# Optimization experiments

Measured on AMD Instinct MI355X. Metric: run time of the kernel, lower is better.

Reference implementation:

```python
import jax, jax.numpy as jnp
import numpy as np

B, L, D, H = 2, 2048, 2048, 16
DH = D // H
SCALE = 1.0 / float(np.sqrt(DH))


def setup_inputs() -> dict:
    key = jax.random.key(0)
    ks = jax.random.split(key, 5)
    std = 1.0 / float(np.sqrt(D))
    return {
        "x": jax.random.normal(ks[0], (B, L, D), dtype=jnp.float32),
        "W_q": jax.random.normal(ks[1], (D, D), dtype=jnp.float32) * std,
        "W_k": jax.random.normal(ks[2], (D, D), dtype=jnp.float32) * std,
        "W_v": jax.random.normal(ks[3], (D, D), dtype=jnp.float32) * std,
        "W_o": jax.random.normal(ks[4], (D, D), dtype=jnp.float32) * std,
    }


def _split_heads(t):
    # (B, L, D) -> (B, H, L, DH)
    b, l, _ = t.shape
    return t.reshape(b, l, H, DH).transpose(0, 2, 1, 3)


def reference(x, W_q, W_k, W_v, W_o):
    # nn.Linear(bias=False): y = x @ W.T
    q = _split_heads(x @ W_q.T)  # (B,H,L,DH)
    k = _split_heads(x @ W_k.T)
    v = _split_heads(x @ W_v.T)
    scores = jnp.einsum("bhqd,bhkd->bhqk", q, k) * SCALE  # (B,H,L,L)
    causal = jnp.arange(L)[:, None] >= jnp.arange(L)[None, :]  # True = keep
    scores = jnp.where(causal[None, None], scores, -jnp.inf)
    attn = jax.nn.softmax(scores, axis=-1)
    y = jnp.einsum("bhqk,bhkd->bhqd", attn, v)  # (B,H,L,DH)
    y = y.transpose(0, 2, 1, 3).reshape(B, L, D)  # merge heads
    return y @ W_o.T
```

## Files before the change

kernel.cpp:

```cpp
#include <hip/hip_runtime.h>
#include <hip/hip_bf16.h>
#include <stdint.h>

typedef unsigned short u16;
typedef __bf16 bf16x8 __attribute__((ext_vector_type(8)));
typedef float f32x4 __attribute__((ext_vector_type(4)));

#define SEQ    2048
#define DMODEL 2048
#define NHEAD  16
#define DHEAD  128
#define QSCALE (0.088388347648318447f * 1.4426950408889634f)

__device__ __forceinline__ u16 f2bf(float f){
  uint32_t u = __float_as_uint(f);
  u += 0x7FFFu + ((u >> 16) & 1u);
  return (u16)(u >> 16);
}

__device__ __forceinline__ void gload_lds16(const u16* g, u16* l){
  __builtin_amdgcn_global_load_lds((const __attribute__((address_space(1))) void*)g,
                                   (__attribute__((address_space(3))) void*)l,
                                   16, 0, 0);
}

__global__ __launch_bounds__(256) void cvt_bf16(const float* __restrict__ src,
                                                u16* __restrict__ dst, int n4){
  int i = blockIdx.x * 256 + threadIdx.x;
  if (i < n4){
    float4 v = reinterpret_cast<const float4*>(src)[i];
    ushort4 o;
    o.x = f2bf(v.x); o.y = f2bf(v.y); o.z = f2bf(v.z); o.w = f2bf(v.w);
    reinterpret_cast<ushort4*>(dst)[i] = o;
  }
}

__global__ __launch_bounds__(256) void cvt_w4(const float* __restrict__ Wq,
    const float* __restrict__ Wk, const float* __restrict__ Wv,
    const float* __restrict__ Wo, u16* __restrict__ dst){
  const int z = blockIdx.y;
  const float* s = (z==0) ? Wq : (z==1) ? Wk : (z==2) ? Wv : Wo;
  int i = blockIdx.x * 256 + threadIdx.x;
  float4 v = reinterpret_cast<const float4*>(s)[i];
  ushort4 o;
  o.x = f2bf(v.x); o.y = f2bf(v.y); o.z = f2bf(v.z); o.w = f2bf(v.w);
  reinterpret_cast<ushort4*>(dst + (size_t)z*4194304)[i] = o;
}

__device__ __forceinline__ void stageA(const u16* __restrict__ G, int grow0, int kt,
                                       int half, u16* lds, int w, int lane){
  #pragma unroll
  for (int j = 0; j < 2; ++j){
    int q   = w*2 + j;
    int r0  = ((q & 8) << 4) + half*64 + (q & 7)*8;
    int row = r0 + (lane >> 3);
    int sc  = (lane & 7) ^ (row & 7);
    gload_lds16(G + (size_t)(grow0 + row)*DMODEL + kt*64 + sc*8, lds + r0*64);
  }
}
__device__ __forceinline__ void stageB(const u16* __restrict__ G, int grow0, int kt,
                                       int half, u16* lds, int w, int lane){
  #pragma unroll
  for (int j = 0; j < 2; ++j){
    int q   = w*2 + j;
    int r0  = ((q >> 2) << 6) + half*32 + (q & 3)*8;
    int row = r0 + (lane >> 3);
    int sc  = (lane & 7) ^ (row & 7);
    gload_lds16(G + (size_t)(grow0 + row)*DMODEL + kt*64 + sc*8, lds + r0*64);
  }
}

__device__ __forceinline__ bf16x8 ldsf(const u16* lds, int row, int c){
  return *reinterpret_cast<const bf16x8*>(lds + row*64 + (((c ^ (row & 7)) & 7) << 3));
}

template<int MH>
__device__ __forceinline__ void load_a(bf16x8 (&a)[4][2], const u16* LA,
                                       int wr, int ln, int g){
  #pragma unroll
  for (int m = 0; m < 4; ++m){
    int row = wr*128 + MH*64 + m*16 + ln;
    a[m][0] = ldsf(LA, row, g);
    a[m][1] = ldsf(LA, row, 4 + g);
  }
}
template<int NH>
__device__ __forceinline__ void load_b(bf16x8 (&b)[2][2], const u16* LB,
                                       int wc, int ln, int g){
  #pragma unroll
  for (int n = 0; n < 2; ++n){
    int row = wc*64 + NH*32 + n*16 + ln;
    b[n][0] = ldsf(LB, row, g);
    b[n][1] = ldsf(LB, row, 4 + g);
  }
}

template<int MH, int NH>
__device__ __forceinline__ void mfma_quad(f32x4 (&acc)[8][4], bf16x8 (&a)[4][2],
                                          bf16x8 (&b)[2][2]){
  __builtin_amdgcn_s_setprio(1);
  #pragma unroll
  for (int m = 0; m < 4; ++m)
    #pragma unroll
    for (int n = 0; n < 2; ++n){
      acc[MH*4+m][NH*2+n] = __builtin_amdgcn_mfma_f32_16x16x32_bf16(
          a[m][0], b[n][0], acc[MH*4+m][NH*2+n], 0, 0, 0);
      acc[MH*4+m][NH*2+n] = __builtin_amdgcn_mfma_f32_16x16x32_bf16(
          a[m][1], b[n][1], acc[MH*4+m][NH*2+n], 0, 0, 0);
    }
  __builtin_amdgcn_s_setprio(0);
}

__device__ __forceinline__ void phase_pre(){
  __builtin_amdgcn_s_barrier();
  asm volatile("s_waitcnt lgkmcnt(0)" ::: "memory");
  __builtin_amdgcn_sched_barrier(0);
}

__device__ __forceinline__ void gemm8_core(const u16* __restrict__ A,
    const u16* __restrict__ W, int bm, int bnl,
    u16 (*ldsA)[256*64], u16 (*ldsB)[256*64], f32x4 (&acc)[8][4],
    int w, int lane, int wr, int wc, int g, int ln){
  const f32x4 z4 = {0.f,0.f,0.f,0.f};
  #pragma unroll
  for (int i = 0; i < 8; ++i)
    #pragma unroll
    for (int j = 0; j < 4; ++j) acc[i][j] = z4;

  stageA(A, bm, 0, 0, ldsA[0], w, lane);
  stageB(W, bnl, 0, 1, ldsB[0], w, lane);
  stageA(A, bm, 0, 1, ldsA[0], w, lane);
  stageB(W, bnl, 0, 0, ldsB[0], w, lane);
  stageA(A, bm, 1, 0, ldsA[1], w, lane);
  stageB(W, bnl, 1, 1, ldsB[1], w, lane);
  asm volatile("s_waitcnt vmcnt(4)" ::: "memory");
  __builtin_amdgcn_s_barrier();

  bf16x8 a[4][2], b[2][2];
  const int NT = DMODEL/64;
  for (int t = 0; t < NT; ++t){
    const int cur = t & 1;
    const u16* LA = ldsA[cur];
    const u16* LB = ldsB[cur];
    load_a<0>(a, LA, wr, ln, g);
    load_b<0>(b, LB, wc, ln, g);
    if (t+1 < NT) stageA(A, bm, t+1, 1, ldsA[cur^1], w, lane);
    phase_pre();
    mfma_quad<0,0>(acc, a, b);
    __builtin_amdgcn_s_barrier();
    load_b<1>(b, LB, wc, ln, g);
    if (t+1 < NT) stageB(W, bnl, t+1, 0, ldsB[cur^1], w, lane);
    phase_pre();
    mfma_quad<0,1>(acc, a, b);
    __builtin_amdgcn_s_barrier();
    load_a<1>(a, LA, wr, ln, g);
    if (t+2 < NT) stageA(A, bm, t+2, 0, ldsA[cur], w, lane);
    phase_pre();
    mfma_quad<1,1>(acc, a, b);
    __builtin_amdgcn_s_barrier();
    load_b<0>(b, LB, wc, ln, g);
    if (t+2 < NT) stageB(W, bnl, t+2, 1, ldsB[cur], w, lane);
    if (t < NT-2) { asm volatile("s_waitcnt vmcnt(4)" ::: "memory"); }
    else          { asm volatile("s_waitcnt vmcnt(0)" ::: "memory"); }
    phase_pre();
    mfma_quad<1,0>(acc, a, b);
    __builtin_amdgcn_s_barrier();
  }
}

__global__ __launch_bounds__(512, 2) void gemm_qkv8(const u16* __restrict__ A,
    const u16* __restrict__ Wall, u16* __restrict__ Q, u16* __restrict__ Kb,
    u16* __restrict__ Vt){
  __shared__ __align__(16) u16 ldsA[2][256*64];
  __shared__ __align__(16) u16 ldsB[2][256*64];
  const int tid = threadIdx.x, w = tid >> 6, lane = tid & 63;
  const int g = lane >> 4, ln = lane & 15;
  const int wr = w >> 2, wc = w & 3;
  const int bid = blockIdx.x;
  const int swz = (bid & 7)*48 + (bid >> 3);
  const int nt = swz >> 4, mt = swz & 15;
  const int bm = mt*256, z = nt >> 3, bnl = (nt & 7) << 8;
  const u16* W = Wall + ((size_t)z << 22);
  f32x4 acc[8][4];
  gemm8_core(A, W, bm, bnl, ldsA, ldsB, acc, w, lane, wr, wc, g, ln);

  if (z < 2){
    u16* C = (z == 0) ? Q : Kb;
    const float sc = (z == 0) ? QSCALE : 1.0f;
    #pragma unroll
    for (int mf = 0; mf < 8; ++mf)
      #pragma unroll
      for (int nf = 0; nf < 4; ++nf){
        int col = bnl + wc*64 + nf*16 + ln;
        #pragma unroll
        for (int i = 0; i < 4; ++i){
          int row = bm + wr*128 + mf*16 + g*4 + i;
          C[(size_t)row*DMODEL + col] = f2bf(acc[mf][nf][i] * sc);
        }
      }
  } else {
    #pragma unroll
    for (int mf = 0; mf < 8; ++mf)
      #pragma unroll
      for (int nf = 0; nf < 4; ++nf){
        int col  = bnl + wc*64 + nf*16 + ln;
        int row0 = bm + wr*128 + mf*16 + g*4;
        int bb   = row0 >> 11, lt = row0 & (SEQ-1);
        ushort4 pk;
        pk.x = f2bf(acc[mf][nf][0]); pk.y = f2bf(acc[mf][nf][1]);
        pk.z = f2bf(acc[mf][nf][2]); pk.w = f2bf(acc[mf][nf][3]);
        *reinterpret_cast<ushort4*>(Vt + (size_t)(bb*DMODEL + col)*SEQ + lt) = pk;
      }
  }
}

__device__ __forceinline__ void stageB2(const u16* __restrict__ G, int grow0,
    int kt, int half, u16* lds, int w, int lane){
  int r0  = half*64 + (w & 7)*8;
  int row = r0 + (lane >> 3);
  int sc  = (lane & 7) ^ (row & 7);
  gload_lds16(G + (size_t)(grow0 + row)*DMODEL + kt*64 + sc*8, lds + r0*64);
}

template<int NH>
__device__ __forceinline__ void load_b2(bf16x8 (&b)[2], const u16* LB,
                                        int wc, int ln, int g){
  int row = NH*64 + wc*16 + ln;
  b[0] = ldsf(LB, row, g);
  b[1] = ldsf(LB, row, 4 + g);
}

template<int MH, int NH>
__device__ __forceinline__ void mfma_oct(f32x4 (&acc)[8][2], bf16x8 (&a)[4][2],
                                         bf16x8 (&b)[2]){
  __builtin_amdgcn_s_setprio(1);
  #pragma unroll
  for (int m = 0; m < 4; ++m){
    acc[MH*4+m][NH] = __builtin_amdgcn_mfma_f32_16x16x32_bf16(
        a[m][0], b[0], acc[MH*4+m][NH], 0, 0, 0);
    acc[MH*4+m][NH] = __builtin_amdgcn_mfma_f32_16x16x32_bf16(
        a[m][1], b[1], acc[MH*4+m][NH], 0, 0, 0);
  }
  __builtin_amdgcn_s_setprio(0);
}

__global__ __launch_bounds__(512, 2) void gemm_out2(const u16* __restrict__ A,
    const u16* __restrict__ Wo, float* __restrict__ C){
  __shared__ __align__(16) u16 ldsA[2][256*64];
  __shared__ __align__(16) u16 ldsB[2][128*64];
  const int tid = threadIdx.x, w = tid >> 6, lane = tid & 63;
  const int g = lane >> 4, ln = lane & 15;
  const int wr = w >> 2, wc = w & 3;
  const int bid = blockIdx.x;
  const int swz = (bid & 7)*32 + (bid >> 3);
  const int nt = swz >> 4, mt = swz & 15;
  const int bm = mt*256, bnl = nt << 7;
  f32x4 acc[8][2];
  {
    const f32x4 z4 = {0.f,0.f,0.f,0.f};
    #pragma unroll
    for (int i = 0; i < 8; ++i){ acc[i][0] = z4; acc[i][1] = z4; }
  }
  stageA (A,  bm,  0, 0, ldsA[0], w, lane);
  stageA (A,  bm,  0, 1, ldsA[0], w, lane);
  stageB2(Wo, bnl, 0, 0, ldsB[0], w, lane);
  stageB2(Wo, bnl, 0, 1, ldsB[0], w, lane);
  stageA (A,  bm,  1, 0, ldsA[1], w, lane);
  stageB2(Wo, bnl, 1, 1, ldsB[1], w, lane);
  asm volatile("s_waitcnt vmcnt(3)" ::: "memory");
  __builtin_amdgcn_s_barrier();

  bf16x8 a[4][2], b0[2], b1[2];
  const int NT = DMODEL/64;
  for (int t = 0; t < NT; ++t){
    const int cur = t & 1;
    const u16* LA = ldsA[cur];
    const u16* LB = ldsB[cur];
    load_a<0>(a, LA, wr, ln, g);
    load_b2<0>(b0, LB, wc, ln, g);
    if (t+1 < NT) stageA(A, bm, t+1, 1, ldsA[cur^1], w, lane);
    phase_pre();
    mfma_oct<0,0>(acc, a, b0);
    __builtin_amdgcn_s_barrier();
    load_b2<1>(b1, LB, wc, ln, g);
    if (t+1 < NT) stageB2(Wo, bnl, t+1, 0, ldsB[cur^1], w, lane);
    phase_pre();
    mfma_oct<0,1>(acc, a, b1);
    __builtin_amdgcn_s_barrier();
    load_a<1>(a, LA, wr, ln, g);
    if (t+2 < NT) stageA(A, bm, t+2, 0, ldsA[cur], w, lane);
    phase_pre();
    mfma_oct<1,1>(acc, a, b1);
    __builtin_amdgcn_s_barrier();
    load_b2<0>(b0, LB, wc, ln, g);
    if (t+2 < NT) stageB2(Wo, bnl, t+2, 1, ldsB[cur], w, lane);
    if (t < NT-2) { asm volatile("s_waitcnt vmcnt(3)" ::: "memory"); }
    else          { asm volatile("s_waitcnt vmcnt(0)" ::: "memory"); }
    phase_pre();
    mfma_oct<1,0>(acc, a, b0);
    __builtin_amdgcn_s_barrier();
  }

  #pragma unroll
  for (int mf = 0; mf < 8; ++mf)
    #pragma unroll
    for (int nf = 0; nf < 2; ++nf){
      int col = bnl + nf*64 + wc*16 + ln;
      #pragma unroll
      for (int i = 0; i < 4; ++i){
        int row = bm + wr*128 + mf*16 + g*4 + i;
        C[(size_t)row*DMODEL + col] = acc[mf][nf][i];
      }
    }
}

__device__ __forceinline__ void attn_stageK(const u16* __restrict__ Kb,
    u16* Kt, int b, int h, int kb, int w, int lane){
  #pragma unroll
  for (int is = 0; is < 4; ++is){
    int o = w*4096 + is*1024 + lane*16;
    int row = o >> 8;
    int sc  = ((o >> 4) & 15) ^ (row & 7);
    gload_lds16(Kb + (size_t)(b*SEQ + kb + row)*DMODEL + h*DHEAD + sc*8,
                Kt + w*2048 + is*512);
  }
}
__device__ __forceinline__ void attn_stageV(const u16* __restrict__ Vtb,
    u16* Vt, int bh, int kb, int w, int lane){
  #pragma unroll
  for (int is = 0; is < 4; ++is){
    int o = w*4096 + is*1024 + lane*16;
    int row = o >> 7;
    int sc  = ((o >> 4) & 7) ^ (row & 7);
    gload_lds16(Vtb + (size_t)(bh*DHEAD + row)*SEQ + kb + sc*8,
                Vt + w*2048 + is*512);
  }
}

template<bool MASKED>
__device__ __forceinline__ void attn_qkt_sm(const u16* Kt, u16* Pw,
    const bf16x8 (&qf)[2][4], f32x4 (&yacc)[2][8],
    float (&mrun)[2], float (&lrun)[2],
    int kb, int qg0, int g, int ln){
  #pragma unroll
  for (int qc = 0; qc < 2; ++qc){
    f32x4 st[4];
    __builtin_amdgcn_s_setprio(1);
    #pragma unroll
    for (int kt = 0; kt < 4; ++kt){
      f32x4 accs = {0.f,0.f,0.f,0.f};
      #pragma unroll
      for (int c = 0; c < 4; ++c){
        int row = kt*16 + ln;
        int ch  = (c*4 + g) ^ (row & 7);
        bf16x8 kf = *reinterpret_cast<const bf16x8*>(Kt + row*128 + ch*8);
        accs = __builtin_amdgcn_mfma_f32_16x16x32_bf16(kf, qf[qc][c], accs, 0, 0, 0);
      }
      st[kt] = accs;
    }
    __builtin_amdgcn_s_setprio(0);

    const int qg = qg0 + qc*16;
    float p[16];
    float tmax = -1e30f;
    #pragma unroll
    for (int kt = 0; kt < 4; ++kt)
      #pragma unroll
      for (int i = 0; i < 4; ++i){
        float s = st[kt][i];
        if (MASKED && (kb + kt*16 + g*4 + i) > qg) s = -1e30f;
        p[kt*4+i] = s;
        tmax = fmaxf(tmax, s);
      }
    tmax = fmaxf(tmax, __shfl_xor(tmax, 16));
    tmax = fmaxf(tmax, __shfl_xor(tmax, 32));

    if (!__all(tmax - mrun[qc] <= 11.5f)){
      float mn = fmaxf(mrun[qc], tmax);
      float fr = __builtin_amdgcn_exp2f(mrun[qc] - mn);
      lrun[qc] *= fr;
      float fi[4];
      #pragma unroll
      for (int i = 0; i < 4; ++i) fi[i] = __shfl(fr, g*4 + i);
      #pragma unroll
      for (int dt = 0; dt < 8; ++dt)
        #pragma unroll
        for (int i = 0; i < 4; ++i) yacc[qc][dt][i] *= fi[i];
      mrun[qc] = mn;
    }
    float psum = 0.f;
    #pragma unroll
    for (int j = 0; j < 16; ++j){
      p[j] = __builtin_amdgcn_exp2f(p[j] - mrun[qc]);
      psum += p[j];
    }
    psum += __shfl_xor(psum, 16);
    psum += __shfl_xor(psum, 32);
    lrun[qc] += psum;

    char* pb = reinterpret_cast<char*>(Pw + qc*1024);
    #pragma unroll
    for (int kt = 0; kt < 4; ++kt)
      #pragma unroll
      for (int pr = 0; pr < 2; ++pr){
        uint32_t pk = (uint32_t)f2bf(p[kt*4 + 2*pr]) |
                      ((uint32_t)f2bf(p[kt*4 + 2*pr + 1]) << 16);
        int byte = (kt*16 + g*4 + 2*pr)*2;
        int ch   = (byte >> 4) ^ (ln & 7);
        int addr = ln*128 + (ch << 4) + (byte & 15);
        *reinterpret_cast<uint32_t*>(pb + addr) = pk;
      }
  }
}

__device__ __forceinline__ void attn_pv(const u16* Vt, const u16* Pw,
                                        f32x4 (&yacc)[2][8], int g, int ln){
  __builtin_amdgcn_s_setprio(1);
  #pragma unroll
  for (int kc = 0; kc < 2; ++kc){
    int chp = (kc*4 + g) ^ (ln & 7);
    bf16x8 pf0 = *reinterpret_cast<const bf16x8*>(Pw +        ln*64 + chp*8);
    bf16x8 pf1 = *reinterpret_cast<const bf16x8*>(Pw + 1024 + ln*64 + chp*8);
    #pragma unroll
    for (int dt = 0; dt < 8; ++dt){
      int row = dt*16 + ln;
      int chv = (kc*4 + g) ^ (row & 7);
      bf16x8 vf = *reinterpret_cast<const bf16x8*>(Vt + row*64 + chv*8);
      yacc[0][dt] = __builtin_amdgcn_mfma_f32_16x16x32_bf16(pf0, vf, yacc[0][dt], 0, 0, 0);
      yacc[1][dt] = __builtin_amdgcn_mfma_f32_16x16x32_bf16(pf1, vf, yacc[1][dt], 0, 0, 0);
    }
  }
  __builtin_amdgcn_s_setprio(0);
}

__global__ __launch_bounds__(256, 2) void attn_fwd(const u16* __restrict__ Qb,
    const u16* __restrict__ Kb, const u16* __restrict__ Vtb, u16* __restrict__ Yb){
  __shared__ __align__(16) u16 Kt[2][64*128];
  __shared__ __align__(16) u16 Vt[2][128*64];
  __shared__ __align__(16) u16 Pl[4][2048];
  const int tid = threadIdx.x, w = tid >> 6, lane = tid & 63;
  const int g = lane >> 4, ln = lane & 15;
  const int bh = blockIdx.y;
  const int b = bh >> 4, h = bh & 15;
  const int qb = (bh < 16) ? blockIdx.x : (15 - blockIdx.x);
  const int qw = qb*128 + w*32;
  const int qg0 = qw + ln;
  const int NT = 2*qb + 2;

  bf16x8 qf[2][4];
  #pragma unroll
  for (int qc = 0; qc < 2; ++qc){
    const u16* qp = Qb + (size_t)(b*SEQ + qw + qc*16 + ln)*DMODEL + h*DHEAD + g*8;
    #pragma unroll
    for (int c = 0; c < 4; ++c) qf[qc][c] = *reinterpret_cast<const bf16x8*>(qp + c*32);
  }
  float mrun[2] = {-1e30f, -1e30f}, lrun[2] = {0.f, 0.f};
  f32x4 yacc[2][8];
  {
    const f32x4 z4 = {0.f,0.f,0.f,0.f};
    #pragma unroll
    for (int qc = 0; qc < 2; ++qc)
      #pragma unroll
      for (int dt = 0; dt < 8; ++dt) yacc[qc][dt] = z4;
  }
  u16* Pw = &Pl[w][0];

  attn_stageK(Kb, &Kt[0][0], b, h, 0, w, lane);
  attn_stageV(Vtb, &Vt[0][0], bh, 0, w, lane);
  asm volatile("s_waitcnt vmcnt(0)" ::: "memory");
  __builtin_amdgcn_s_barrier();

  int cur = 0;
  for (int t = 0; t < NT; ++t){
    const int kb = t*64;
    if (t+1 < NT){
      attn_stageK(Kb, &Kt[cur^1][0], b, h, kb + 64, w, lane);
      attn_stageV(Vtb, &Vt[cur^1][0], bh, kb + 64, w, lane);
    }
    if (t < NT-2)
      attn_qkt_sm<false>(&Kt[cur][0], Pw, qf, yacc, mrun, lrun, kb, qg0, g, ln);
    else
      attn_qkt_sm<true >(&Kt[cur][0], Pw, qf, yacc, mrun, lrun, kb, qg0, g, ln);
    attn_pv(&Vt[cur][0], Pw, yacc, g, ln);
    asm volatile("s_waitcnt vmcnt(0) lgkmcnt(0)" ::: "memory");
    __builtin_amdgcn_s_barrier();
    cur ^= 1;
  }

  #pragma unroll
  for (int qc = 0; qc < 2; ++qc){
    float inv[4];
    #pragma unroll
    for (int i = 0; i < 4; ++i){
      float li = __shfl(lrun[qc], g*4 + i);
      inv[i] = __builtin_amdgcn_rcpf(li);
    }
    #pragma unroll
    for (int dt = 0; dt < 8; ++dt)
      #pragma unroll
      for (int i = 0; i < 4; ++i){
        Yb[(size_t)(b*SEQ + qw + qc*16 + g*4 + i)*DMODEL + h*DHEAD + dt*16 + ln] =
            f2bf(yacc[qc][dt][i] * inv[i]);
      }
  }
}

extern "C" void kernel_launch(void* const* d_in, const int* in_sizes, int n_in,
                              void* d_out, int out_size, void* d_ws, size_t ws_size,
                              hipStream_t stream) {
  const float* x  = (const float*)d_in[0];
  const float* Wq = (const float*)d_in[1];
  const float* Wk = (const float*)d_in[2];
  const float* Wv = (const float*)d_in[3];
  const float* Wo = (const float*)d_in[4];
  float* out = (float*)d_out;

  char* ws = (char*)d_ws;
  u16* xb  = (u16*)(ws +          0);
  u16* Wqb = (u16*)(ws + 16777216);
  u16* Wob = (u16*)(ws + 41943040);
  u16* Qb  = (u16*)(ws + 50331648);
  u16* Kb  = (u16*)(ws + 67108864);
  u16* Vtb = (u16*)(ws + 83886080);
  u16* Yb  = (u16*)(ws + 100663296);

  cvt_bf16<<<dim3(8192), 256, 0, stream>>>(x, xb, 2097152);
  cvt_w4<<<dim3(4096, 4), 256, 0, stream>>>(Wq, Wk, Wv, Wo, Wqb);

  gemm_qkv8<<<dim3(384), 512, 0, stream>>>(xb, Wqb, Qb, Kb, Vtb);

  attn_fwd<<<dim3(16, 32), 256, 0, stream>>>(Qb, Kb, Vtb, Yb);

  gemm_out2<<<dim3(256), 512, 0, stream>>>(Yb, Wob, out);
}
```

Baseline: 290.6 us.

## Merge conversion kernels, restructure out-proj pipeline, skip masked attention tiles per wave

The x and weight fp32-to-bf16 conversions are merged into one launch. The output-projection GEMM is restructured into two MFMA phases per k-step instead of four, with fewer barriers, a different B staging and fragment layout, and a new block-to-tile mapping. The attention loop also lets waves whose queries lie wholly before the last key tiles skip those fully masked tiles, which removes wasted QK^T and PV work. The trade-offs are higher register pressure from the larger B fragment set and less interleaving of loads with compute in the GEMM.

```diff
diff --git a/kernel.cpp b/kernel.cpp
--- a/kernel.cpp
+++ b/kernel.cpp
@@ -24,27 +24,22 @@
                                    16, 0, 0);
 }
 
-__global__ __launch_bounds__(256) void cvt_bf16(const float* __restrict__ src,
-                                                u16* __restrict__ dst, int n4){
-  int i = blockIdx.x * 256 + threadIdx.x;
-  if (i < n4){
-    float4 v = reinterpret_cast<const float4*>(src)[i];
-    ushort4 o;
-    o.x = f2bf(v.x); o.y = f2bf(v.y); o.z = f2bf(v.z); o.w = f2bf(v.w);
-    reinterpret_cast<ushort4*>(dst)[i] = o;
-  }
-}
-
-__global__ __launch_bounds__(256) void cvt_w4(const float* __restrict__ Wq,
-    const float* __restrict__ Wk, const float* __restrict__ Wv,
-    const float* __restrict__ Wo, u16* __restrict__ dst){
-  const int z = blockIdx.y;
-  const float* s = (z==0) ? Wq : (z==1) ? Wk : (z==2) ? Wv : Wo;
-  int i = blockIdx.x * 256 + threadIdx.x;
-  float4 v = reinterpret_cast<const float4*>(s)[i];
+__global__ __launch_bounds__(256) void cvt_all(const float* __restrict__ x,
+    const float* __restrict__ Wq, const float* __restrict__ Wk,
+    const float* __restrict__ Wv, const float* __restrict__ Wo,
+    u16* __restrict__ dst){
+  int gid = blockIdx.x * 256 + threadIdx.x;
+  const float* s; int idx;
+  if (gid < 2097152){ s = x; idx = gid; }
+  else {
+    int j = gid - 2097152;
+    int z = j >> 20; idx = j & 0xFFFFF;
+    s = (z==0) ? Wq : (z==1) ? Wk : (z==2) ? Wv : Wo;
+  }
+  float4 v = reinterpret_cast<const float4*>(s)[idx];
   ushort4 o;
   o.x = f2bf(v.x); o.y = f2bf(v.y); o.z = f2bf(v.z); o.w = f2bf(v.w);
-  reinterpret_cast<ushort4*>(dst + (size_t)z*4194304)[i] = o;
+  reinterpret_cast<ushort4*>(dst)[gid] = o;
 }
 
 __device__ __forceinline__ void stageA(const u16* __restrict__ G, int grow0, int kt,
@@ -214,37 +209,45 @@
   }
 }
 
-__device__ __forceinline__ void stageB2(const u16* __restrict__ G, int grow0,
-    int kt, int half, u16* lds, int w, int lane){
-  int r0  = half*64 + (w & 7)*8;
-  int row = r0 + (lane >> 3);
-  int sc  = (lane & 7) ^ (row & 7);
-  gload_lds16(G + (size_t)(grow0 + row)*DMODEL + kt*64 + sc*8, lds + r0*64);
-}
-
-template<int NH>
-__device__ __forceinline__ void load_b2(bf16x8 (&b)[2], const u16* LB,
+__device__ __forceinline__ void stageB3(const u16* __restrict__ G, int grow0,
+    int kt, u16* lds, int w, int lane){
+  #pragma unroll
+  for (int j = 0; j < 2; ++j){
+    int q   = w*2 + j;
+    int r0  = q*8;
+    int row = r0 + (lane >> 3);
+    int sc  = (lane & 7) ^ (row & 7);
+    gload_lds16(G + (size_t)(grow0 + row)*DMODEL + kt*64 + sc*8, lds + r0*64);
+  }
+}
+
+__device__ __forceinline__ void load_b3(bf16x8 (&b)[2][2], const u16* LB,
                                         int wc, int ln, int g){
-  int row = NH*64 + wc*16 + ln;
-  b[0] = ldsf(LB, row, g);
-  b[1] = ldsf(LB, row, 4 + g);
-}
-
-template<int MH, int NH>
-__device__ __forceinline__ void mfma_oct(f32x4 (&acc)[8][2], bf16x8 (&a)[4][2],
-                                         bf16x8 (&b)[2]){
+  #pragma unroll
+  for (int n = 0; n < 2; ++n){
+    int row = wc*32 + n*16 + ln;
+    b[n][0] = ldsf(LB, row, g);
+    b[n][1] = ldsf(LB, row, 4 + g);
+  }
+}
+
+template<int MH>
+__device__ __forceinline__ void mfma8x2(f32x4 (&acc)[8][2], bf16x8 (&a)[4][2],
+                                        bf16x8 (&b)[2][2]){
   __builtin_amdgcn_s_setprio(1);
   #pragma unroll
-  for (int m = 0; m < 4; ++m){
-    acc[MH*4+m][NH] = __builtin_amdgcn_mfma_f32_16x16x32_bf16(
-        a[m][0], b[0], acc[MH*4+m][NH], 0, 0, 0);
-    acc[MH*4+m][NH] = __builtin_amdgcn_mfma_f32_16x16x32_bf16(
-        a[m][1], b[1], acc[MH*4+m][NH], 0, 0, 0);
-  }
+  for (int m = 0; m < 4; ++m)
+    #pragma unroll
+    for (int n = 0; n < 2; ++n){
+      acc[MH*4+m][n] = __builtin_amdgcn_mfma_f32_16x16x32_bf16(
+          a[m][0], b[n][0], acc[MH*4+m][n], 0, 0, 0);
+      acc[MH*4+m][n] = __builtin_amdgcn_mfma_f32_16x16x32_bf16(
+          a[m][1], b[n][1], acc[MH*4+m][n], 0, 0, 0);
+    }
   __builtin_amdgcn_s_setprio(0);
 }
 
-__global__ __launch_bounds__(512, 2) void gemm_out2(const u16* __restrict__ A,
+__global__ __launch_bounds__(512, 2) void gemm_out3(const u16* __restrict__ A,
     const u16* __restrict__ Wo, float* __restrict__ C){
   __shared__ __align__(16) u16 ldsA[2][256*64];
   __shared__ __align__(16) u16 ldsB[2][128*64];
@@ -252,8 +255,8 @@
   const int g = lane >> 4, ln = lane & 15;
   const int wr = w >> 2, wc = w & 3;
   const int bid = blockIdx.x;
-  const int swz = (bid & 7)*32 + (bid >> 3);
-  const int nt = swz >> 4, mt = swz & 15;
+  const int x = bid & 7, s = bid >> 3;
+  const int mt = s >> 1, nt = 2*x + (s & 1);
   const int bm = mt*256, bnl = nt << 7;
   f32x4 acc[8][2];
   {
@@ -263,41 +266,32 @@
   }
   stageA (A,  bm,  0, 0, ldsA[0], w, lane);
   stageA (A,  bm,  0, 1, ldsA[0], w, lane);
-  stageB2(Wo, bnl, 0, 0, ldsB[0], w, lane);
-  stageB2(Wo, bnl, 0, 1, ldsB[0], w, lane);
+  stageB3(Wo, bnl, 0,    ldsB[0], w, lane);
   stageA (A,  bm,  1, 0, ldsA[1], w, lane);
-  stageB2(Wo, bnl, 1, 1, ldsB[1], w, lane);
-  asm volatile("s_waitcnt vmcnt(3)" ::: "memory");
+  asm volatile("s_waitcnt vmcnt(2)" ::: "memory");
   __builtin_amdgcn_s_barrier();
 
-  bf16x8 a[4][2], b0[2], b1[2];
+  bf16x8 a[4][2], b[2][2];
   const int NT = DMODEL/64;
   for (int t = 0; t < NT; ++t){
     const int cur = t & 1;
     const u16* LA = ldsA[cur];
     const u16* LB = ldsB[cur];
     load_a<0>(a, LA, wr, ln, g);
-    load_b2<0>(b0, LB, wc, ln, g);
-    if (t+1 < NT) stageA(A, bm, t+1, 1, ldsA[cur^1], w, lane);
+    load_b3(b, LB, wc, ln, g);
+    if (t+1 < NT){
+      stageA (A,  bm,  t+1, 1, ldsA[cur^1], w, lane);
+      stageB3(Wo, bnl, t+1,    ldsB[cur^1], w, lane);
+    }
     phase_pre();
-    mfma_oct<0,0>(acc, a, b0);
-    __builtin_amdgcn_s_barrier();
-    load_b2<1>(b1, LB, wc, ln, g);
-    if (t+1 < NT) stageB2(Wo, bnl, t+1, 0, ldsB[cur^1], w, lane);
-    phase_pre();
-    mfma_oct<0,1>(acc, a, b1);
+    mfma8x2<0>(acc, a, b);
     __builtin_amdgcn_s_barrier();
     load_a<1>(a, LA, wr, ln, g);
     if (t+2 < NT) stageA(A, bm, t+2, 0, ldsA[cur], w, lane);
-    phase_pre();
-    mfma_oct<1,1>(acc, a, b1);
-    __builtin_amdgcn_s_barrier();
-    load_b2<0>(b0, LB, wc, ln, g);
-    if (t+2 < NT) stageB2(Wo, bnl, t+2, 1, ldsB[cur], w, lane);
-    if (t < NT-2) { asm volatile("s_waitcnt vmcnt(3)" ::: "memory"); }
+    if (t < NT-2) { asm volatile("s_waitcnt vmcnt(2)" ::: "memory"); }
     else          { asm volatile("s_waitcnt vmcnt(0)" ::: "memory"); }
     phase_pre();
-    mfma_oct<1,0>(acc, a, b0);
+    mfma8x2<1>(acc, a, b);
     __builtin_amdgcn_s_barrier();
   }
 
@@ -305,7 +299,7 @@
   for (int mf = 0; mf < 8; ++mf)
     #pragma unroll
     for (int nf = 0; nf < 2; ++nf){
-      int col = bnl + nf*64 + wc*16 + ln;
+      int col = bnl + wc*32 + nf*16 + ln;
       #pragma unroll
       for (int i = 0; i < 4; ++i){
         int row = bm + wr*128 + mf*16 + g*4 + i;
@@ -477,11 +471,17 @@
       attn_stageK(Kb, &Kt[cur^1][0], b, h, kb + 64, w, lane);
       attn_stageV(Vtb, &Vt[cur^1][0], bh, kb + 64, w, lane);
     }
-    if (t < NT-2)
+    bool active = true;
+    if (t < NT-2){
       attn_qkt_sm<false>(&Kt[cur][0], Pw, qf, yacc, mrun, lrun, kb, qg0, g, ln);
-    else
-      attn_qkt_sm<true >(&Kt[cur][0], Pw, qf, yacc, mrun, lrun, kb, qg0, g, ln);
-    attn_pv(&Vt[cur][0], Pw, yacc, g, ln);
+    } else if (t == NT-2){
+      if (w >= 2) attn_qkt_sm<false>(&Kt[cur][0], Pw, qf, yacc, mrun, lrun, kb, qg0, g, ln);
+      else        attn_qkt_sm<true >(&Kt[cur][0], Pw, qf, yacc, mrun, lrun, kb, qg0, g, ln);
+    } else {
+      if (w >= 2) attn_qkt_sm<true >(&Kt[cur][0], Pw, qf, yacc, mrun, lrun, kb, qg0, g, ln);
+      else        active = false;
+    }
+    if (active) attn_pv(&Vt[cur][0], Pw, yacc, g, ln);
     asm volatile("s_waitcnt vmcnt(0) lgkmcnt(0)" ::: "memory");
     __builtin_amdgcn_s_barrier();
     cur ^= 1;
@@ -524,12 +524,11 @@
   u16* Vtb = (u16*)(ws + 83886080);
   u16* Yb  = (u16*)(ws + 100663296);
 
-  cvt_bf16<<<dim3(8192), 256, 0, stream>>>(x, xb, 2097152);
-  cvt_w4<<<dim3(4096, 4), 256, 0, stream>>>(Wq, Wk, Wv, Wo, Wqb);
+  cvt_all<<<dim3(24576), 256, 0, stream>>>(x, Wq, Wk, Wv, Wo, xb);
 
   gemm_qkv8<<<dim3(384), 512, 0, stream>>>(xb, Wqb, Qb, Kb, Vtb);
 
   attn_fwd<<<dim3(16, 32), 256, 0, stream>>>(Qb, Kb, Vtb, Yb);
 
-  gemm_out2<<<dim3(256), 512, 0, stream>>>(Yb, Wob, out);
-}
+  gemm_out3<<<dim3(256), 512, 0, stream>>>(Yb, Wob, out);
+}
```

Result: faster. 276.9 us (-4.7%).
